# Kernel tuning notes

Hardware: AMD Instinct MI355X
Metric: run time of the kernel (lower is better)

## Reference

```python
import jax, jax.numpy as jnp
import numpy as np

B, N, C = 8, 4096, 256
HEADS, SR = 8, 4
LN_EPS = 1e-5

def setup_inputs() -> dict:
    key = jax.random.key(0)
    ks = jax.random.split(key, 8)
    std = 0.02
    x = jax.random.normal(ks[0], (B, N, C), dtype=jnp.float32)
    q_w = jax.random.normal(ks[1], (C, C), dtype=jnp.float32) * std          # [in,out]
    kv_w = jax.random.normal(ks[2], (C, 2 * C), dtype=jnp.float32) * std     # [in,2*out]
    fan_out = SR * SR * C
    sr_w = jax.random.normal(ks[3], (C, C, SR, SR), dtype=jnp.float32) * np.sqrt(2.0 / fan_out)  # OIHW
    sr_b = jnp.zeros((C,), dtype=jnp.float32)
    ln_w = jnp.ones((C,), dtype=jnp.float32)
    ln_b = jnp.zeros((C,), dtype=jnp.float32)
    proj_w = jax.random.normal(ks[4], (C, C), dtype=jnp.float32) * std
    proj_b = jnp.zeros((C,), dtype=jnp.float32)
    return {"x": x, "H": 64, "W": 64, "q_w": q_w, "kv_w": kv_w, "sr_w": sr_w,
            "sr_b": sr_b, "ln_w": ln_w, "ln_b": ln_b, "proj_w": proj_w, "proj_b": proj_b}


def reference(x, H, W, q_w, kv_w, sr_w, sr_b, ln_w, ln_b, proj_w, proj_b):
    Bb, Nn, Cc = x.shape
    hd = Cc // HEADS
    scale = hd ** -0.5
    # q: [B, heads, N, hd]
    q = (x @ q_w).reshape(Bb, Nn, HEADS, hd).transpose(0, 2, 1, 3)
    # spatial reduction: conv(stride=sr) + LayerNorm
    x_ = x.transpose(0, 2, 1).reshape(Bb, Cc, H, W)
    x_ = jax.lax.conv_general_dilated(
        x_, sr_w, window_strides=(SR, SR), padding="VALID",
        dimension_numbers=("NCHW", "OIHW", "NCHW")) + sr_b[None, :, None, None]
    x_ = x_.reshape(Bb, Cc, -1).transpose(0, 2, 1)  # [B, Nk, C]
    mu = x_.mean(-1, keepdims=True)
    var = x_.var(-1, keepdims=True)
    x_ = (x_ - mu) * jax.lax.rsqrt(var + LN_EPS) * ln_w + ln_b
    # kv: [B, Nk, 2, heads, hd]
    Nk = x_.shape[1]
    kv = (x_ @ kv_w).reshape(Bb, Nk, 2, HEADS, hd)
    k = kv[:, :, 0].transpose(0, 2, 1, 3)  # [B, heads, Nk, hd]
    v = kv[:, :, 1].transpose(0, 2, 1, 3)  # [B, heads, Nk, hd]
    attn = jnp.einsum("bhnd,bhmd->bhnm", q, k) * scale
    attn = jax.nn.softmax(attn, axis=-1)
    out = jnp.einsum("bhnm,bhmd->bhnd", attn, v)  # [B, heads, N, hd]
    out = out.transpose(0, 2, 1, 3).reshape(Bb, Nn, Cc)
    return out @ proj_w + proj_b
```

## Files before the change

### kernel.cpp

```cpp
#include <hip/hip_runtime.h>
#include <hip/hip_bf16.h>
#include <math.h>

#define DI __device__ __forceinline__

static constexpr float SCALE = 0.17677669529663687f;

typedef short bf16x8 __attribute__((ext_vector_type(8)));
typedef float f32x4 __attribute__((ext_vector_type(4)));

__device__ unsigned short g_qw2[(size_t)256 * 8 * 64];
__device__ unsigned short g_kvw2[(size_t)512 * 8 * 64];
__device__ unsigned short g_pw2[(size_t)256 * 8 * 64];
__device__ unsigned short g_wt2[(size_t)256 * 128 * 64];
__device__ unsigned short g_x2[(size_t)32768 * 8 * 64];
__device__ unsigned short g_ln2[(size_t)2048 * 8 * 64];
__device__ unsigned short g_q[(size_t)64 * 4096 * 32];
__device__ unsigned short g_k[(size_t)64 * 256 * 32];
__device__ unsigned short g_vt[(size_t)64 * 32 * 256];
__device__ unsigned short g_convp[(size_t)16 * 2048 * 256];
__device__ unsigned short g_attnb[(size_t)32768 * 256];

DI float bfbits2f(unsigned short b) { return __uint_as_float(((unsigned)b) << 16); }

DI unsigned short f2bf(float f) {
  unsigned u = __float_as_uint(f);
  unsigned r = (u + 0x7fffu + ((u >> 16) & 1u)) >> 16;
  return (unsigned short)r;
}

DI float4 ld_bf4(const unsigned short* p) {
  ushort4 u = *(const ushort4*)p;
  return make_float4(bfbits2f(u.x), bfbits2f(u.y), bfbits2f(u.z), bfbits2f(u.w));
}

DI float ld1(const void* p, size_t i, int f32) {
  return f32 ? ((const float*)p)[i] : bfbits2f(((const unsigned short*)p)[i]);
}

DI float4 ld4(const void* p, size_t i, int f32) {
  if (f32) return *(const float4*)((const float*)p + i);
  return ld_bf4((const unsigned short*)p + i);
}

typedef const __attribute__((address_space(1))) void* gas_p;
typedef __attribute__((address_space(3))) void* las_p;
DI void gload16(const unsigned short* g, short* l) {
  __builtin_amdgcn_global_load_lds((gas_p)g, (las_p)l, 16, 0, 0);
}

template <int N> DI void wait_vmcnt() {
  if constexpr (N == 6) asm volatile("s_waitcnt vmcnt(6)" ::: "memory");
  else if constexpr (N == 5) asm volatile("s_waitcnt vmcnt(5)" ::: "memory");
  else if constexpr (N == 4) asm volatile("s_waitcnt vmcnt(4)" ::: "memory");
  else asm volatile("s_waitcnt vmcnt(0)" ::: "memory");
}

DI int detect_f32(const void* xp) {
  const unsigned* p = (const unsigned*)xp;
  unsigned m0 = 0, m1 = 0;
#pragma unroll
  for (int i = 0; i < 32; ++i) {
    unsigned w = p[i];
    unsigned lo = w & 0x7fffu, hi = (w >> 16) & 0x7fffu;
    m0 = lo > m0 ? lo : m0;
    m1 = hi > m1 ? hi : m1;
  }
  unsigned mm = m0 > m1 ? m0 : m1;
  return mm >= 0x4680u ? 1 : 0;
}

__global__ void k_prep(const void* __restrict__ qw, const void* __restrict__ kvw,
                       const void* __restrict__ pwp, const void* __restrict__ srw,
                       const void* __restrict__ xp) {
  const int f32 = detect_f32(xp);
  int tidg = blockIdx.x * 256 + threadIdx.x;
  float v[8];
  unsigned short* dst;
  if (tidg < 8192) {
    int o = tidg >> 5, w = tidg & 31, k = w * 8;
#pragma unroll
    for (int j = 0; j < 8; ++j) v[j] = ld1(qw, (size_t)(k + j) * 256 + o, f32) * SCALE;
    dst = g_qw2 + ((size_t)o * 8 + (w >> 2)) * 64 + (w & 3) * 8;
  } else if (tidg < 24576) {
    int t = tidg - 8192;
    int o = t >> 5, w = t & 31, k = w * 8;
#pragma unroll
    for (int j = 0; j < 8; ++j) v[j] = ld1(kvw, (size_t)(k + j) * 512 + o, f32);
    dst = g_kvw2 + ((size_t)o * 8 + (w >> 2)) * 64 + (w & 3) * 8;
  } else if (tidg < 32768) {
    int t = tidg - 24576;
    int o = t >> 5, w = t & 31, k = w * 8;
#pragma unroll
    for (int j = 0; j < 8; ++j) v[j] = ld1(pwp, (size_t)(k + j) * 256 + o, f32);
    dst = g_pw2 + ((size_t)o * 8 + (w >> 2)) * 64 + (w & 3) * 8;
  } else if (tidg < 163840) {
    int t = tidg - 32768;
    int o = t >> 9, w = t & 511, k = w * 8;
#pragma unroll
    for (int j = 0; j < 8; ++j) {
      int kk = k + j, tap = kk >> 8, ci = kk & 255;
      v[j] = ld1(srw, (size_t)o * 4096 + (size_t)ci * 16 + tap, f32);
    }
    dst = g_wt2 + ((size_t)o * 128 + (w >> 2)) * 64 + (w & 3) * 8;
  } else {
    int t = tidg - 163840;
    int m = t >> 5, w = t & 31, k = w * 8;
    size_t base = (size_t)m * 256 + k;
    float4 a = ld4(xp, base, f32);
    float4 b = ld4(xp, base + 4, f32);
    v[0] = a.x; v[1] = a.y; v[2] = a.z; v[3] = a.w;
    v[4] = b.x; v[5] = b.y; v[6] = b.z; v[7] = b.w;
    dst = g_x2 + ((size_t)m * 8 + (w >> 2)) * 64 + (w & 3) * 8;
  }
  ushort4 h0, h1, l0, l1;
  h0.x = f2bf(v[0]); l0.x = f2bf(v[0] - bfbits2f(h0.x));
  h0.y = f2bf(v[1]); l0.y = f2bf(v[1] - bfbits2f(h0.y));
  h0.z = f2bf(v[2]); l0.z = f2bf(v[2] - bfbits2f(h0.z));
  h0.w = f2bf(v[3]); l0.w = f2bf(v[3] - bfbits2f(h0.w));
  h1.x = f2bf(v[4]); l1.x = f2bf(v[4] - bfbits2f(h1.x));
  h1.y = f2bf(v[5]); l1.y = f2bf(v[5] - bfbits2f(h1.y));
  h1.z = f2bf(v[6]); l1.z = f2bf(v[6] - bfbits2f(h1.z));
  h1.w = f2bf(v[7]); l1.w = f2bf(v[7] - bfbits2f(h1.w));
  *(ushort4*)dst        = h0;
  *(ushort4*)(dst + 4)  = h1;
  *(ushort4*)(dst + 32) = l0;
  *(ushort4*)(dst + 36) = l1;
}

template <int MODE>
DI void mgemm_body(short* smem, int bx, int nblk, int z,
                   const void* __restrict__ biasp, void* __restrict__ outp, int f32) {
  constexpr bool AH = (MODE != 3);
  constexpr int BN  = (MODE == 2) ? 64 : 128;
  constexpr int NJ  = BN / 64;
  constexpr int NBR = BN / 32;
  constexpr int ASZ = AH ? 4096 : 2048;
  constexpr int BSZ = NBR * 2048;
  constexpr int BUF = ASZ + BSZ;
  constexpr int NLD = (AH ? 2 : 1) + NBR;
  constexpr int NIT = (MODE == 1) ? 32 : 8;
  constexpr int NKT = (MODE == 1) ? 128 : 8;

  const int tid = threadIdx.x;
  const int m0 = bx * 64;
  const int wave = tid >> 6, lane = tid & 63;
  const int quad = lane >> 4, l15 = lane & 15;

  const int srow = tid >> 3;
  const int slot = (tid & 7) ^ (srow & 7);

  size_t arow0 = 0, arow1 = 0, abase3 = 0;
  if constexpr (MODE == 0 || MODE == 2) {
    arow0 = m0 + srow;
    arow1 = m0 + 32 + srow;
  } else if constexpr (MODE == 1) {
#pragma unroll
    for (int r = 0; r < 2; ++r) {
      int m = m0 + r * 32 + srow;
      int bb = m >> 8, sp = m & 255;
      int oh = sp >> 4, ow = sp & 15;
      size_t rb = (size_t)bb * 4096 + (4 * oh + z) * 64 + 4 * ow;
      if (r == 0) arow0 = rb; else arow1 = rb;
    }
  } else {
    int ar = tid >> 2;
    int s3 = (tid & 3) ^ (ar & 3);
    abase3 = (size_t)(m0 + ar) * 256 + s3 * 8;
  }

  const unsigned short* Asrc =
      (MODE == 0 || MODE == 1) ? g_x2 : (MODE == 2) ? g_ln2 : g_attnb;
  const unsigned short* Bsrc = (MODE == 0) ? g_qw2 : (MODE == 1) ? g_wt2
                             : (MODE == 2) ? g_kvw2 : g_pw2;
  const int brow0 = nblk * BN + srow;

  int aoff[4], boff[NJ];
#pragma unroll
  for (int mt = 0; mt < 4; ++mt) {
    int ar = mt * 16 + l15;
    if constexpr (AH) aoff[mt] = ar * 64 + ((quad ^ (ar & 7)) << 3);
    else              aoff[mt] = ar * 32 + ((quad ^ (ar & 3)) << 3);
  }
#pragma unroll
  for (int j = 0; j < NJ; ++j) {
    int br = wave * (16 * NJ) + j * 16 + l15;
    boff[j] = br * 64 + ((quad ^ (br & 7)) << 3);
  }

  auto STAGE = [&](int it, int b) {
    short* sa = smem + b * BUF;
    short* sb = sa + ASZ;
    if constexpr (MODE == 0 || MODE == 2) {
      gload16(Asrc + (arow0 * 8 + it) * 64 + slot * 8, sa + tid * 8);
      gload16(Asrc + (arow1 * 8 + it) * 64 + slot * 8, sa + 2048 + tid * 8);
    } else if constexpr (MODE == 1) {
      const int kw = it >> 3, ktA = it & 7;
      gload16(Asrc + ((arow0 + kw) * 8 + ktA) * 64 + slot * 8, sa + tid * 8);
      gload16(Asrc + ((arow1 + kw) * 8 + ktA) * 64 + slot * 8, sa + 2048 + tid * 8);
    } else {
      gload16(Asrc + abase3 + (size_t)it * 32, sa + tid * 8);
    }
    const int ktB = (MODE == 1) ? (z * 32 + it) : it;
#pragma unroll
    for (int r = 0; r < NBR; ++r)
      gload16(Bsrc + ((size_t)(brow0 + r * 32) * NKT + ktB) * 64 + slot * 8,
              sb + tid * 8 + r * 2048);
  };

  f32x4 acc[4][NJ] = {};

  auto COMPUTE = [&](int cur) {
    const short* sa = smem + cur * BUF;
    const short* sb = sa + ASZ;
#pragma unroll
    for (int mt = 0; mt < 4; ++mt) {
      bf16x8 a_h = *(const bf16x8*)&sa[aoff[mt]];
      bf16x8 a_l;
      if constexpr (AH) a_l = *(const bf16x8*)&sa[aoff[mt] ^ 32];
#pragma unroll
      for (int j = 0; j < NJ; ++j) {
        bf16x8 b_h = *(const bf16x8*)&sb[boff[j]];
        bf16x8 b_l = *(const bf16x8*)&sb[boff[j] ^ 32];
        f32x4 c = acc[mt][j];
        c = __builtin_amdgcn_mfma_f32_16x16x32_bf16(a_h, b_h, c, 0, 0, 0);
        if constexpr (AH)
          c = __builtin_amdgcn_mfma_f32_16x16x32_bf16(a_l, b_h, c, 0, 0, 0);
        c = __builtin_amdgcn_mfma_f32_16x16x32_bf16(a_h, b_l, c, 0, 0, 0);
        acc[mt][j] = c;
      }
    }
  };

  STAGE(0, 0);
  STAGE(1, 1);
#pragma unroll 1
  for (int it = 0; it < NIT - 1; ++it) {
    const int cur = it & 1;
    wait_vmcnt<NLD>();
    __builtin_amdgcn_s_barrier();
    __builtin_amdgcn_sched_barrier(0);
    COMPUTE(cur);
    asm volatile("" ::: "memory");
    __builtin_amdgcn_s_barrier();
    __builtin_amdgcn_sched_barrier(0);
    if (it < NIT - 2) STAGE(it + 2, cur);
  }
  wait_vmcnt<0>();
  __builtin_amdgcn_s_barrier();
  __builtin_amdgcn_sched_barrier(0);
  COMPUTE((NIT - 1) & 1);

  const int f32o = f32;
#pragma unroll
  for (int mt = 0; mt < 4; ++mt) {
#pragma unroll
    for (int j = 0; j < NJ; ++j) {
#pragma unroll
      for (int r = 0; r < 4; ++r) {
        int m = m0 + mt * 16 + quad * 4 + r;
        int c = nblk * BN + wave * (16 * NJ) + j * 16 + l15;
        float v = acc[mt][j][r];
        if constexpr (MODE == 0) {
          int b = m >> 12, n = m & 4095;
          int h = c >> 5, d = c & 31;
          g_q[(((size_t)(b * 8 + h) * 4096 + n) << 5) + d] = f2bf(v);
        } else if constexpr (MODE == 1) {
          g_convp[((size_t)z * 2048 + m) * 256 + c] = f2bf(v);
        } else if constexpr (MODE == 2) {
          int s = c >> 8, h = (c >> 5) & 7, d = c & 31;
          int bb = m >> 8, nk = m & 255;
          if (s == 0) {
            g_k[(((size_t)(bb * 8 + h) * 256 + nk) << 5) + d] = f2bf(v);
          } else {
            int w = nk & 31, cb = nk & ~31;
            int ww = w & 15;
            int vslot = cb + ((ww >> 2) << 3) + ((w >> 4) << 2) + (ww & 3);
            g_vt[(((size_t)(bb * 8 + h) * 32 + d) << 8) + vslot] = f2bf(v);
          }
        } else {
          float rr = v + ld1(biasp, c, f32o);
          if (f32o) ((float*)outp)[(size_t)m * 256 + c] = rr;
          else      ((unsigned short*)outp)[(size_t)m * 256 + c] = f2bf(rr);
        }
      }
    }
  }
}

__launch_bounds__(256, 3)
__global__ void k_mgemm01() {
  __shared__ __align__(16) short smem[2 * 12288];
  int bid = blockIdx.x;
  if (bid < 256) {
    int m = bid & 31, nb = (bid >> 5) & 1, z = bid >> 6;
    mgemm_body<1>(smem, m, nb, z, nullptr, nullptr, 0);
  } else {
    int bq = bid - 256;
    int lq = (bq & 7) * 128 + (bq >> 3);
    mgemm_body<0>(smem, lq >> 1, lq & 1, 0, nullptr, nullptr, 0);
  }
}

__launch_bounds__(256, 3)
__global__ void k_mgemm2() {
  __shared__ __align__(16) short smem[2 * 8192];
  int b = blockIdx.x;
  int lq = (b & 7) * 32 + (b >> 3);
  mgemm_body<2>(smem, lq >> 3, lq & 7, 0, nullptr, nullptr, 0);
}

__launch_bounds__(256, 4)
__global__ void k_mgemm3(const void* __restrict__ xp, const void* __restrict__ pb,
                         void* __restrict__ outp) {
  __shared__ __align__(16) short smem[2 * 10240];
  int lq = ((int)blockIdx.x & 7) * 128 + ((int)blockIdx.x >> 3);
  mgemm_body<3>(smem, lq >> 1, lq & 1, 0, pb, outp, detect_f32(xp));
}

__global__ void k_redln(const void* __restrict__ xp, const void* __restrict__ srb,
                        const void* __restrict__ lw, const void* __restrict__ lb) {
  const int f32 = detect_f32(xp);
  const int t = threadIdx.x;
  const int row = blockIdx.x * 8 + (t >> 5);
  const int l32 = t & 31;
  const int ch0 = l32 * 8;
  const size_t idx = (size_t)row * 256 + ch0;

  float c[8] = {};
#pragma unroll
  for (int zz = 0; zz < 4; ++zz) {
    uint4 u = *(const uint4*)&g_convp[(size_t)zz * (2048 * 256) + idx];
    c[0] += __uint_as_float(u.x << 16); c[1] += __uint_as_float(u.x & 0xffff0000u);
    c[2] += __uint_as_float(u.y << 16); c[3] += __uint_as_float(u.y & 0xffff0000u);
    c[4] += __uint_as_float(u.z << 16); c[5] += __uint_as_float(u.z & 0xffff0000u);
    c[6] += __uint_as_float(u.w << 16); c[7] += __uint_as_float(u.w & 0xffff0000u);
  }
  float4 b0 = ld4(srb, ch0, f32), b1 = ld4(srb, ch0 + 4, f32);
  c[0] += b0.x; c[1] += b0.y; c[2] += b0.z; c[3] += b0.w;
  c[4] += b1.x; c[5] += b1.y; c[6] += b1.z; c[7] += b1.w;

  float s = 0.f, sq = 0.f;
#pragma unroll
  for (int j = 0; j < 8; ++j) { s += c[j]; sq += c[j] * c[j]; }
#pragma unroll
  for (int off = 16; off >= 1; off >>= 1) {
    s += __shfl_xor(s, off, 32);
    sq += __shfl_xor(sq, off, 32);
  }
  float mu = s * (1.0f / 256.0f);
  float var = sq * (1.0f / 256.0f) - mu * mu;
  float rr = rsqrtf(var + 1e-5f);

  float4 w0 = ld4(lw, ch0, f32), w1 = ld4(lw, ch0 + 4, f32);
  float4 e0 = ld4(lb, ch0, f32), e1 = ld4(lb, ch0 + 4, f32);
  float wv[8] = {w0.x, w0.y, w0.z, w0.w, w1.x, w1.y, w1.z, w1.w};
  float ev[8] = {e0.x, e0.y, e0.z, e0.w, e1.x, e1.y, e1.z, e1.w};

  float o[8];
#pragma unroll
  for (int j = 0; j < 8; ++j) o[j] = (c[j] - mu) * rr * wv[j] + ev[j];

  ushort4 h0, h1, l0, l1;
  h0.x = f2bf(o[0]); l0.x = f2bf(o[0] - bfbits2f(h0.x));
  h0.y = f2bf(o[1]); l0.y = f2bf(o[1] - bfbits2f(h0.y));
  h0.z = f2bf(o[2]); l0.z = f2bf(o[2] - bfbits2f(h0.z));
  h0.w = f2bf(o[3]); l0.w = f2bf(o[3] - bfbits2f(h0.w));
  h1.x = f2bf(o[4]); l1.x = f2bf(o[4] - bfbits2f(h1.x));
  h1.y = f2bf(o[5]); l1.y = f2bf(o[5] - bfbits2f(h1.y));
  h1.z = f2bf(o[6]); l1.z = f2bf(o[6] - bfbits2f(h1.z));
  h1.w = f2bf(o[7]); l1.w = f2bf(o[7] - bfbits2f(h1.w));

  const size_t dbase = ((size_t)row * 8 + (l32 >> 2)) * 64 + (l32 & 3) * 8;
  *(ushort4*)&g_ln2[dbase]          = h0;
  *(ushort4*)&g_ln2[dbase + 4]      = h1;
  *(ushort4*)&g_ln2[dbase + 32]     = l0;
  *(ushort4*)&g_ln2[dbase + 36]     = l1;
}

__launch_bounds__(256, 4)
__global__ void k_attn() {
  __shared__ short smem[18688];
  short* sk  = smem;
  short* svt = smem + 10240;

  const int tid = threadIdx.x;
  const int bh = blockIdx.y;
  const int b = bh >> 3, h = bh & 7;

  {
    const uint4* gk = (const uint4*)(g_k + (size_t)bh * 8192);
    const uint4* gv = (const uint4*)(g_vt + (size_t)bh * 8192);
    for (int i = tid; i < 1024; i += 256) {
      int key = i >> 2, part = i & 3;
      *(uint4*)&sk[key * 40 + part * 8] = gk[i];
      int d = i >> 5, off = (i & 31) * 8;
      *(uint4*)&svt[d * 264 + off] = gv[i];
    }
  }
  __syncthreads();

  const int wave = tid >> 6, lane = tid & 63;
  const int quad = lane >> 4, l15 = lane & 15;
  const int n0 = blockIdx.x * 64 + wave * 16;

  bf16x8 qv = *(const bf16x8*)(g_q + ((size_t)bh * 4096 + n0 + l15) * 32 + quad * 8);

  f32x4 sacc[16];
  __builtin_amdgcn_s_setprio(1);
#pragma unroll
  for (int t = 0; t < 16; ++t) {
    bf16x8 kf = *(const bf16x8*)&sk[(t * 16 + l15) * 40 + quad * 8];
    f32x4 c = {0.f, 0.f, 0.f, 0.f};
    sacc[t] = __builtin_amdgcn_mfma_f32_16x16x32_bf16(kf, qv, c, 0, 0, 0);
  }
  __builtin_amdgcn_s_setprio(0);

  float m = sacc[0][0];
#pragma unroll
  for (int t = 0; t < 16; ++t) {
#pragma unroll
    for (int r = 0; r < 4; ++r) m = fmaxf(m, sacc[t][r]);
  }
  m = fmaxf(m, __shfl_xor(m, 16, 64));
  m = fmaxf(m, __shfl_xor(m, 32, 64));

  unsigned plo[16], phi[16];
  float ls = 0.f;
#pragma unroll
  for (int t = 0; t < 16; ++t) {
    unsigned short p0 = f2bf(__expf(sacc[t][0] - m));
    unsigned short p1 = f2bf(__expf(sacc[t][1] - m));
    unsigned short p2 = f2bf(__expf(sacc[t][2] - m));
    unsigned short p3 = f2bf(__expf(sacc[t][3] - m));
    ls += bfbits2f(p0) + bfbits2f(p1) + bfbits2f(p2) + bfbits2f(p3);
    plo[t] = (unsigned)p0 | ((unsigned)p1 << 16);
    phi[t] = (unsigned)p2 | ((unsigned)p3 << 16);
  }
  ls += __shfl_xor(ls, 16, 64);
  ls += __shfl_xor(ls, 32, 64);
  float inv = 1.0f / ls;

  f32x4 o0 = {0.f, 0.f, 0.f, 0.f}, o1 = {0.f, 0.f, 0.f, 0.f};
  __builtin_amdgcn_s_setprio(1);
#pragma unroll
  for (int c = 0; c < 8; ++c) {
    uint4 pk = make_uint4(plo[2 * c], phi[2 * c], plo[2 * c + 1], phi[2 * c + 1]);
    bf16x8 pf = *(bf16x8*)&pk;
    bf16x8 v0 = *(const bf16x8*)&svt[l15 * 264 + c * 32 + quad * 8];
    bf16x8 v1 = *(const bf16x8*)&svt[(16 + l15) * 264 + c * 32 + quad * 8];
    o0 = __builtin_amdgcn_mfma_f32_16x16x32_bf16(v0, pf, o0, 0, 0, 0);
    o1 = __builtin_amdgcn_mfma_f32_16x16x32_bf16(v1, pf, o1, 0, 0, 0);
  }
  __builtin_amdgcn_s_setprio(0);

  size_t base = ((size_t)(b * 4096 + n0 + l15)) * 256 + h * 32 + quad * 4;
  ushort4 u0, u1;
  u0.x = f2bf(o0[0] * inv); u0.y = f2bf(o0[1] * inv);
  u0.z = f2bf(o0[2] * inv); u0.w = f2bf(o0[3] * inv);
  u1.x = f2bf(o1[0] * inv); u1.y = f2bf(o1[1] * inv);
  u1.z = f2bf(o1[2] * inv); u1.w = f2bf(o1[3] * inv);
  *(ushort4*)&g_attnb[base]      = u0;
  *(ushort4*)&g_attnb[base + 16] = u1;
}

extern "C" void kernel_launch(void* const* d_in, const int* in_sizes, int n_in,
                              void* d_out, int out_size, void* d_ws, size_t ws_size,
                              hipStream_t stream) {
  const void* x   = d_in[0];
  const void* qw  = d_in[3];
  const void* kvw = d_in[4];
  const void* srw = d_in[5];
  const void* srb = d_in[6];
  const void* lnw = d_in[7];
  const void* lnb = d_in[8];
  const void* pw  = d_in[9];
  const void* pb  = d_in[10];

  k_prep<<<4736, 256, 0, stream>>>(qw, kvw, pw, srw, x);
  k_mgemm01<<<1280, 256, 0, stream>>>();
  k_redln<<<256, 256, 0, stream>>>(x, srb, lnw, lnb);
  k_mgemm2<<<256, 256, 0, stream>>>();
  k_attn<<<dim3(64, 64), 256, 0, stream>>>();
  k_mgemm3<<<1024, 256, 0, stream>>>(x, pb, d_out);
}
```

Baseline: 202.0 us.

## Fuse attention with output projection GEMM via shared-memory attention tile

Merges the attention kernel and the output projection GEMM into one kernel. Each block loops over all 8 heads for a 64-row tile, keeps the bf16 attention output in swizzled LDS, then runs the projection with double-buffered weight staging and writes the final output with bias. This removes the global round-trip of the attention intermediate and one launch. In exchange there are fewer blocks (512 at 2 per CU), heads are processed serially with barriers, and occupancy is lower.

```diff
diff --git a/kernel.cpp b/kernel.cpp
--- a/kernel.cpp
+++ b/kernel.cpp
@@ -310,14 +310,6 @@
   mgemm_body<2>(smem, lq >> 3, lq & 7, 0, nullptr, nullptr, 0);
 }
 
-__launch_bounds__(256, 4)
-__global__ void k_mgemm3(const void* __restrict__ xp, const void* __restrict__ pb,
-                         void* __restrict__ outp) {
-  __shared__ __align__(16) short smem[2 * 10240];
-  int lq = ((int)blockIdx.x & 7) * 128 + ((int)blockIdx.x >> 3);
-  mgemm_body<3>(smem, lq >> 1, lq & 1, 0, pb, outp, detect_f32(xp));
-}
-
 __global__ void k_redln(const void* __restrict__ xp, const void* __restrict__ srb,
                         const void* __restrict__ lw, const void* __restrict__ lb) {
   const int f32 = detect_f32(xp);
@@ -378,90 +370,181 @@
   *(ushort4*)&g_ln2[dbase + 36]     = l1;
 }
 
-__launch_bounds__(256, 4)
-__global__ void k_attn() {
-  __shared__ short smem[18688];
-  short* sk  = smem;
-  short* svt = smem + 10240;
-
+__launch_bounds__(256, 2)
+__global__ void k_attnproj(const void* __restrict__ xp, const void* __restrict__ pb,
+                           void* __restrict__ outp) {
+  __shared__ __align__(16) short smem[16384 + 18688];
+  short* att = smem;
+  short* skv = smem + 16384;
+
+  const int f32o = detect_f32(xp);
   const int tid = threadIdx.x;
-  const int bh = blockIdx.y;
-  const int b = bh >> 3, h = bh & 7;
-
-  {
-    const uint4* gk = (const uint4*)(g_k + (size_t)bh * 8192);
-    const uint4* gv = (const uint4*)(g_vt + (size_t)bh * 8192);
-    for (int i = tid; i < 1024; i += 256) {
-      int key = i >> 2, part = i & 3;
-      *(uint4*)&sk[key * 40 + part * 8] = gk[i];
-      int d = i >> 5, off = (i & 31) * 8;
-      *(uint4*)&svt[d * 264 + off] = gv[i];
-    }
-  }
-  __syncthreads();
+  int lq = ((int)blockIdx.x & 7) * 64 + ((int)blockIdx.x >> 3);
+  const int b = lq >> 6, ntile = lq & 63;
 
   const int wave = tid >> 6, lane = tid & 63;
   const int quad = lane >> 4, l15 = lane & 15;
-  const int n0 = blockIdx.x * 64 + wave * 16;
-
-  bf16x8 qv = *(const bf16x8*)(g_q + ((size_t)bh * 4096 + n0 + l15) * 32 + quad * 8);
-
-  f32x4 sacc[16];
-  __builtin_amdgcn_s_setprio(1);
-#pragma unroll
-  for (int t = 0; t < 16; ++t) {
-    bf16x8 kf = *(const bf16x8*)&sk[(t * 16 + l15) * 40 + quad * 8];
-    f32x4 c = {0.f, 0.f, 0.f, 0.f};
-    sacc[t] = __builtin_amdgcn_mfma_f32_16x16x32_bf16(kf, qv, c, 0, 0, 0);
-  }
-  __builtin_amdgcn_s_setprio(0);
-
-  float m = sacc[0][0];
-#pragma unroll
-  for (int t = 0; t < 16; ++t) {
-#pragma unroll
-    for (int r = 0; r < 4; ++r) m = fmaxf(m, sacc[t][r]);
-  }
-  m = fmaxf(m, __shfl_xor(m, 16, 64));
-  m = fmaxf(m, __shfl_xor(m, 32, 64));
-
-  unsigned plo[16], phi[16];
-  float ls = 0.f;
-#pragma unroll
-  for (int t = 0; t < 16; ++t) {
-    unsigned short p0 = f2bf(__expf(sacc[t][0] - m));
-    unsigned short p1 = f2bf(__expf(sacc[t][1] - m));
-    unsigned short p2 = f2bf(__expf(sacc[t][2] - m));
-    unsigned short p3 = f2bf(__expf(sacc[t][3] - m));
-    ls += bfbits2f(p0) + bfbits2f(p1) + bfbits2f(p2) + bfbits2f(p3);
-    plo[t] = (unsigned)p0 | ((unsigned)p1 << 16);
-    phi[t] = (unsigned)p2 | ((unsigned)p3 << 16);
-  }
-  ls += __shfl_xor(ls, 16, 64);
-  ls += __shfl_xor(ls, 32, 64);
-  float inv = 1.0f / ls;
-
-  f32x4 o0 = {0.f, 0.f, 0.f, 0.f}, o1 = {0.f, 0.f, 0.f, 0.f};
-  __builtin_amdgcn_s_setprio(1);
-#pragma unroll
-  for (int c = 0; c < 8; ++c) {
-    uint4 pk = make_uint4(plo[2 * c], phi[2 * c], plo[2 * c + 1], phi[2 * c + 1]);
-    bf16x8 pf = *(bf16x8*)&pk;
-    bf16x8 v0 = *(const bf16x8*)&svt[l15 * 264 + c * 32 + quad * 8];
-    bf16x8 v1 = *(const bf16x8*)&svt[(16 + l15) * 264 + c * 32 + quad * 8];
-    o0 = __builtin_amdgcn_mfma_f32_16x16x32_bf16(v0, pf, o0, 0, 0, 0);
-    o1 = __builtin_amdgcn_mfma_f32_16x16x32_bf16(v1, pf, o1, 0, 0, 0);
-  }
-  __builtin_amdgcn_s_setprio(0);
-
-  size_t base = ((size_t)(b * 4096 + n0 + l15)) * 256 + h * 32 + quad * 4;
-  ushort4 u0, u1;
-  u0.x = f2bf(o0[0] * inv); u0.y = f2bf(o0[1] * inv);
-  u0.z = f2bf(o0[2] * inv); u0.w = f2bf(o0[3] * inv);
-  u1.x = f2bf(o1[0] * inv); u1.y = f2bf(o1[1] * inv);
-  u1.z = f2bf(o1[2] * inv); u1.w = f2bf(o1[3] * inv);
-  *(ushort4*)&g_attnb[base]      = u0;
-  *(ushort4*)&g_attnb[base + 16] = u1;
+  const int rw = wave * 16 + l15;
+  const int n0g = ntile * 64 + wave * 16;
+
+  short* sk  = skv;
+  short* svt = skv + 10240;
+
+#pragma unroll 1
+  for (int h = 0; h < 8; ++h) {
+    const int bh = b * 8 + h;
+    {
+      const uint4* gk = (const uint4*)(g_k + (size_t)bh * 8192);
+      const uint4* gv = (const uint4*)(g_vt + (size_t)bh * 8192);
+      for (int i = tid; i < 1024; i += 256) {
+        int key = i >> 2, part = i & 3;
+        *(uint4*)&sk[key * 40 + part * 8] = gk[i];
+        int d = i >> 5, off = (i & 31) * 8;
+        *(uint4*)&svt[d * 264 + off] = gv[i];
+      }
+    }
+    __syncthreads();
+
+    bf16x8 qv = *(const bf16x8*)(g_q + ((size_t)bh * 4096 + n0g + l15) * 32 + quad * 8);
+
+    f32x4 sacc[16];
+    __builtin_amdgcn_s_setprio(1);
+#pragma unroll
+    for (int t = 0; t < 16; ++t) {
+      bf16x8 kf = *(const bf16x8*)&sk[(t * 16 + l15) * 40 + quad * 8];
+      f32x4 c = {0.f, 0.f, 0.f, 0.f};
+      sacc[t] = __builtin_amdgcn_mfma_f32_16x16x32_bf16(kf, qv, c, 0, 0, 0);
+    }
+    __builtin_amdgcn_s_setprio(0);
+
+    float m = sacc[0][0];
+#pragma unroll
+    for (int t = 0; t < 16; ++t) {
+#pragma unroll
+      for (int r = 0; r < 4; ++r) m = fmaxf(m, sacc[t][r]);
+    }
+    m = fmaxf(m, __shfl_xor(m, 16, 64));
+    m = fmaxf(m, __shfl_xor(m, 32, 64));
+
+    unsigned plo[16], phi[16];
+    float ls = 0.f;
+#pragma unroll
+    for (int t = 0; t < 16; ++t) {
+      unsigned short p0 = f2bf(__expf(sacc[t][0] - m));
+      unsigned short p1 = f2bf(__expf(sacc[t][1] - m));
+      unsigned short p2 = f2bf(__expf(sacc[t][2] - m));
+      unsigned short p3 = f2bf(__expf(sacc[t][3] - m));
+      ls += bfbits2f(p0) + bfbits2f(p1) + bfbits2f(p2) + bfbits2f(p3);
+      plo[t] = (unsigned)p0 | ((unsigned)p1 << 16);
+      phi[t] = (unsigned)p2 | ((unsigned)p3 << 16);
+    }
+    ls += __shfl_xor(ls, 16, 64);
+    ls += __shfl_xor(ls, 32, 64);
+    float inv = 1.0f / ls;
+
+    f32x4 o0 = {0.f, 0.f, 0.f, 0.f}, o1 = {0.f, 0.f, 0.f, 0.f};
+    __builtin_amdgcn_s_setprio(1);
+#pragma unroll
+    for (int c = 0; c < 8; ++c) {
+      uint4 pk = make_uint4(plo[2 * c], phi[2 * c], plo[2 * c + 1], phi[2 * c + 1]);
+      bf16x8 pf = *(bf16x8*)&pk;
+      bf16x8 v0 = *(const bf16x8*)&svt[l15 * 264 + c * 32 + quad * 8];
+      bf16x8 v1 = *(const bf16x8*)&svt[(16 + l15) * 264 + c * 32 + quad * 8];
+      o0 = __builtin_amdgcn_mfma_f32_16x16x32_bf16(v0, pf, o0, 0, 0, 0);
+      o1 = __builtin_amdgcn_mfma_f32_16x16x32_bf16(v1, pf, o1, 0, 0, 0);
+    }
+    __builtin_amdgcn_s_setprio(0);
+
+    ushort4 u0, u1;
+    u0.x = f2bf(o0[0] * inv); u0.y = f2bf(o0[1] * inv);
+    u0.z = f2bf(o0[2] * inv); u0.w = f2bf(o0[3] * inv);
+    u1.x = f2bf(o1[0] * inv); u1.y = f2bf(o1[1] * inv);
+    u1.z = f2bf(o1[2] * inv); u1.w = f2bf(o1[3] * inv);
+    int s0 = h * 4 + (quad >> 1);
+    int woff = (quad & 1) * 4;
+    *(ushort4*)&att[rw * 256 + (((s0    ) ^ (rw & 7)) << 3) + woff] = u0;
+    *(ushort4*)&att[rw * 256 + (((s0 + 2) ^ (rw & 7)) << 3) + woff] = u1;
+    __syncthreads();
+  }
+
+  const int srow = tid >> 3;
+  const int slot = (tid & 7) ^ (srow & 7);
+
+  auto STAGE_B = [&](int s) {
+    short* sb = skv + (s & 1) * 8192;
+    int nb = s >> 3, it = s & 7;
+    int brow0 = nb * 128 + srow;
+#pragma unroll
+    for (int r = 0; r < 4; ++r)
+      gload16(g_pw2 + ((size_t)(brow0 + r * 32) * 8 + it) * 64 + slot * 8,
+              sb + tid * 8 + r * 2048);
+  };
+
+  int boff[2];
+#pragma unroll
+  for (int j = 0; j < 2; ++j) {
+    int br = wave * 32 + j * 16 + l15;
+    boff[j] = br * 64 + ((quad ^ (br & 7)) << 3);
+  }
+
+  f32x4 acc[4][2] = {};
+
+  auto PCOMP = [&](int s) {
+    const short* sb = skv + (s & 1) * 8192;
+    int it = s & 7;
+#pragma unroll
+    for (int mt = 0; mt < 4; ++mt) {
+      int ar = mt * 16 + l15;
+      bf16x8 a_h = *(const bf16x8*)&att[ar * 256 + (((it * 4 + quad) ^ (ar & 7)) << 3)];
+#pragma unroll
+      for (int j = 0; j < 2; ++j) {
+        bf16x8 b_h = *(const bf16x8*)&sb[boff[j]];
+        bf16x8 b_l = *(const bf16x8*)&sb[boff[j] ^ 32];
+        f32x4 c = acc[mt][j];
+        c = __builtin_amdgcn_mfma_f32_16x16x32_bf16(a_h, b_h, c, 0, 0, 0);
+        c = __builtin_amdgcn_mfma_f32_16x16x32_bf16(a_h, b_l, c, 0, 0, 0);
+        acc[mt][j] = c;
+      }
+    }
+  };
+
+  auto EPI = [&](int nb) {
+#pragma unroll
+    for (int mt = 0; mt < 4; ++mt) {
+#pragma unroll
+      for (int j = 0; j < 2; ++j) {
+#pragma unroll
+        for (int r = 0; r < 4; ++r) {
+          int m = ntile * 64 + mt * 16 + quad * 4 + r;
+          int c = nb * 128 + wave * 32 + j * 16 + l15;
+          float v = acc[mt][j][r] + ld1(pb, c, f32o);
+          if (f32o) ((float*)outp)[((size_t)b * 4096 + m) * 256 + c] = v;
+          else ((unsigned short*)outp)[((size_t)b * 4096 + m) * 256 + c] = f2bf(v);
+          acc[mt][j][r] = 0.f;
+        }
+      }
+    }
+  };
+
+  STAGE_B(0);
+  STAGE_B(1);
+#pragma unroll 1
+  for (int s = 0; s < 15; ++s) {
+    wait_vmcnt<4>();
+    __builtin_amdgcn_s_barrier();
+    __builtin_amdgcn_sched_barrier(0);
+    PCOMP(s);
+    asm volatile("" ::: "memory");
+    __builtin_amdgcn_s_barrier();
+    __builtin_amdgcn_sched_barrier(0);
+    if (s < 14) STAGE_B(s + 2);
+    if (s == 7) EPI(0);
+  }
+  wait_vmcnt<0>();
+  __builtin_amdgcn_s_barrier();
+  __builtin_amdgcn_sched_barrier(0);
+  PCOMP(15);
+  EPI(1);
 }
 
 extern "C" void kernel_launch(void* const* d_in, const int* in_sizes, int n_in,
@@ -481,6 +564,5 @@
   k_mgemm01<<<1280, 256, 0, stream>>>();
   k_redln<<<256, 256, 0, stream>>>(x, srb, lnw, lnb);
   k_mgemm2<<<256, 256, 0, stream>>>();
-  k_attn<<<dim3(64, 64), 256, 0, stream>>>();
-  k_mgemm3<<<1024, 256, 0, stream>>>(x, pb, d_out);
-}
+  k_attnproj<<<512, 256, 0, stream>>>(x, pb, d_out);
+}
```

Result: no change. 202.1 us (+0.0%).
